# Optimization experiments

Hardware: AMD Instinct MI355X
Metric: run time of the kernel (lower is better)

The kernel has to match this reference:

```python
import jax, jax.numpy as jnp
import numpy as np

# ---- hardcoded module constants (from Cyborg.__init__) ----
B, S, V = 256, 128, 512
H = 30              # number of symbol vectors
N_STACKS = 2
R = 2               # REDUNDANCY
DEPTH = 4           # stack_depth
ZERO_OFFSET = 1e-6
NAND_BIAS = 3.0
INIT_SHARPEN = 10.0
N_VECS = 1 + N_STACKS  # input vec + one peek per stack = 3
C_BIG = (H + N_STACKS) * R   # 64 choices for push_fn / calc_out
C_SMALL = 2 * R              # 4 choices for pop_op / push_op


def _cossim(a, b, eps=1e-8):
    # torch.cosine_similarity semantics: per-vector norm clamp
    na = jnp.maximum(jnp.linalg.norm(a, axis=-1, keepdims=True), eps)
    nb = jnp.maximum(jnp.linalg.norm(b, axis=-1, keepdims=True), eps)
    return jnp.sum((a / na) * (b / nb), axis=-1)


def _nand(query, w, nw_raw):
    # Fuzzy-NAND gate bank (neurallambda NAND, clip='abs').
    # query: [B, N_VECS*V], w: [C, N_VECS*V], nw_raw: [C, N_VECS] -> [B, C]
    C = w.shape[0]
    q = query.reshape(-1, 1, N_VECS, V)
    wv = w.reshape(1, C, N_VECS, V)
    cos = jnp.abs(_cossim(q, wv))                 # [B, C, N_VECS], clip='abs'
    nw = jax.nn.sigmoid(nw_raw)[None]             # interpolate sim vs NOT(sim)
    interp = nw * cos + (1.0 - nw) * (1.0 - cos)
    return jnp.prod(interp, axis=-1)              # fuzzy AND over the 3 vecs


# ---- differentiable stack (soft pointer over DEPTH slots) ----
def _read(stack, ptr):
    return jnp.einsum('bdv,bd->bv', stack, ptr)

def _push(stack, ptr, val):
    p = jnp.roll(ptr, 1, axis=1)
    s = stack * (1.0 - p)[..., None] + val[:, None, :] * p[..., None]
    return s, p

def _pop(stack, ptr):
    s = stack * (1.0 - ptr)[..., None] + ZERO_OFFSET * ptr[..., None]
    p = jnp.roll(ptr, -1, axis=1)
    return s, p

def _pop_or_nop(stack, ptr, sharp, should_pop, should_nop):
    pr = jax.nn.softmax(jnp.stack([should_pop, should_nop], -1) * sharp, axis=-1)
    ps, pp = _pop(stack, ptr)
    s = ps * pr[:, 0, None, None] + stack * pr[:, 1, None, None]
    p = pp * pr[:, 0, None] + ptr * pr[:, 1, None]
    return s, p

def _push_or_nop(stack, ptr, sharp, should_push, should_nop, val):
    pr = jax.nn.softmax(jnp.stack([should_push, should_nop], -1) * sharp, axis=-1)
    ps, pp = _push(stack, ptr, val)
    s = ps * pr[:, 0, None, None] + stack * pr[:, 1, None, None]
    p = pp * pr[:, 0, None] + ptr * pr[:, 1, None]
    return s, p


def _forward(x, syms, stack_init_vec, sharp, pop_w, pop_nw, pushop_w, pushop_nw,
             pushfn_w, pushfn_nw, calc_w, calc_nw):
    b = x.shape[0]
    # init both stacks to zero_offset, pointer at slot 0, then hard-push init vec
    stack0 = jnp.full((N_STACKS, b, DEPTH, V), ZERO_OFFSET, x.dtype)
    ptr0 = jnp.zeros((N_STACKS, b, DEPTH), x.dtype).at[:, :, 0].set(1.0)
    init_val = jnp.broadcast_to(stack_init_vec, (b, V))
    stack0, ptr0 = jax.vmap(_push, in_axes=(0, 0, None))(stack0, ptr0, init_val)

    syms_b = jnp.broadcast_to(syms, (b, H, V))

    def step(carry, inp):
        stacks, ptrs = carry                                    # [2,B,D,V], [2,B,D]
        peeks = jax.vmap(_read)(stacks, ptrs)                   # [2,B,V]
        inps = jnp.concatenate([inp, peeks[0], peeks[1]], -1)   # [B,3V]
        out_opts = jnp.concatenate(
            [syms_b, peeks[0][:, None], peeks[1][:, None]], 1)  # [B,H+2,V]
        new_s, new_p = [], []
        for k in range(N_STACKS):
            pops = _nand(inps, pop_w[k], pop_nw[k])             # [B, 2R]
            pushes = _nand(inps, pushop_w[k], pushop_nw[k])     # [B, 2R]
            pv = _nand(inps, pushfn_w[k], pushfn_nw[k]).reshape(b, H + N_STACKS, R)
            push_val = jnp.einsum('bcv,bcr->bv', out_opts, pv)
            s, p = _pop_or_nop(stacks[k], ptrs[k], sharp[k],
                               pops[:, :R].max(1), pops[:, R:].max(1))
            s, p = _push_or_nop(s, p, sharp[k],
                                pushes[:, :R].max(1), pushes[:, R:].max(1), push_val)
            new_s.append(s)
            new_p.append(p)
        stacks = jnp.stack(new_s)
        ptrs = jnp.stack(new_p)
        peeks2 = jax.vmap(_read)(stacks, ptrs)
        inps2 = jnp.concatenate([inp, peeks2[0], peeks2[1]], -1)
        out_opts2 = jnp.concatenate(
            [syms_b, peeks2[0][:, None], peeks2[1][:, None]], 1)
        cv = _nand(inps2, calc_w, calc_nw).reshape(b, H + N_STACKS, R)
        out = jnp.einsum('bcv,bcr->bv', out_opts2, cv)
        return (stacks, ptrs), out

    _, outs = jax.lax.scan(step, (stack0, ptr0), jnp.swapaxes(x, 0, 1))
    return jnp.swapaxes(outs, 0, 1)  # [B,S,V]


def setup_inputs() -> dict:
    key = jax.random.key(0)
    ks = jax.random.split(key, 12)
    siv = jax.random.normal(ks[1], (V,), jnp.float32)
    siv = siv / jnp.linalg.norm(siv)
    return {
        'x': jax.random.normal(ks[0], (B, S, V), jnp.float32),
        'syms': jax.random.normal(ks[2], (H, V), jnp.float32),
        'stack_init_vec': siv,
        'sharp': jnp.full((N_STACKS,), INIT_SHARPEN, jnp.float32),
        'pop_w': jax.random.normal(ks[3], (N_STACKS, C_SMALL, N_VECS * V), jnp.float32),
        'pop_nw': jax.random.normal(ks[4], (N_STACKS, C_SMALL, N_VECS), jnp.float32) + NAND_BIAS,
        'pushop_w': jax.random.normal(ks[5], (N_STACKS, C_SMALL, N_VECS * V), jnp.float32),
        'pushop_nw': jax.random.normal(ks[6], (N_STACKS, C_SMALL, N_VECS), jnp.float32) + NAND_BIAS,
        'pushfn_w': jax.random.normal(ks[7], (N_STACKS, C_BIG, N_VECS * V), jnp.float32),
        'pushfn_nw': jax.random.normal(ks[8], (N_STACKS, C_BIG, N_VECS), jnp.float32) + NAND_BIAS,
        'calc_w': jax.random.normal(ks[9], (C_BIG, N_VECS * V), jnp.float32),
        'calc_nw': jax.random.normal(ks[10], (C_BIG, N_VECS), jnp.float32) + NAND_BIAS,
    }


def reference(x, syms, stack_init_vec, sharp, pop_w, pop_nw, pushop_w, pushop_nw,
              pushfn_w, pushfn_nw, calc_w, calc_nw):
    return _forward(x, syms, stack_init_vec, sharp, pop_w, pop_nw, pushop_w,
                    pushop_nw, pushfn_w, pushfn_nw, calc_w, calc_nw)
```

## Files before the change

kernel.cpp:

```cpp
#include <hip/hip_runtime.h>
#include <math.h>


#define SS 128
#define VV 512
#define NROWS 208
#define ZOFF 1e-6f

#define OFF_I0   0
#define OFF_OC   (32768*208)
#define OFF_GI   (OFF_OC + 32768*32)
#define OFF_M    (OFF_GI + 2*32*208)
#define OFF_A    (OFF_M + 1024)
#define OFF_Bc   (OFF_A + 624)
#define OFF_W0   (OFF_Bc + 624)

typedef _Float16 half8 __attribute__((ext_vector_type(8)));
typedef float f32x4 __attribute__((ext_vector_type(4)));

__device__ __forceinline__ float rlane(float v, int lane) {
    return __int_as_float(__builtin_amdgcn_readlane(__float_as_int(v), lane));
}
template <int CTRL>
__device__ __forceinline__ float dpp_add(float x) {
    int y = __builtin_amdgcn_update_dpp(0, __float_as_int(x), CTRL, 0xF, 0xF, true);
    return x + __int_as_float(y);
}
__device__ __forceinline__ float sum16(float x) {
    x = dpp_add<0xB1>(x);
    x = dpp_add<0x4E>(x);
    x = dpp_add<0x124>(x);
    x = dpp_add<0x128>(x);
    return x;
}
__device__ __forceinline__ float swz16(float x) {
    return __int_as_float(__builtin_amdgcn_ds_swizzle(__float_as_int(x), 0x401F));
}

__device__ __forceinline__ const float* w_row(int r, const float* pw, const float* pow_,
                                              const float* pfw, const float* cw) {
    if (r < 8)   return pw   + r * 1536;
    if (r < 16)  return pow_ + (r - 8) * 1536;
    if (r < 144) return pfw  + (r - 16) * 1536;
    return cw + (r - 144) * 1536;
}
__device__ __forceinline__ const float* nw_row(int r, const float* pn, const float* pon,
                                               const float* pfn, const float* cn) {
    if (r < 8)   return pn   + r * 3;
    if (r < 16)  return pon  + (r - 8) * 3;
    if (r < 144) return pfn  + (r - 16) * 3;
    return cn + (r - 144) * 3;
}

__global__ void kB(const float* __restrict__ syms, const float* __restrict__ siv,
                   const float* __restrict__ pw, const float* __restrict__ pn,
                   const float* __restrict__ pow_, const float* __restrict__ pon,
                   const float* __restrict__ pfw, const float* __restrict__ pfn,
                   const float* __restrict__ cw, const float* __restrict__ cn,
                   float* __restrict__ ws) {
    int blk = blockIdx.x, tid = threadIdx.x;
    if (blk < 64) {
        int jj = blk >> 5, e = blk & 31;
        __shared__ float bas[512];
        for (int i = tid; i < 512; i += 256)
            bas[i] = (e == 0) ? 1.0f : ((e == 1) ? siv[i] : syms[(e - 2) * 512 + i]);
        __syncthreads();
        if (tid < NROWS) {
            int c = tid;
            const float4* w4 = (const float4*)(w_row(c, pw, pow_, pfw, cw) + (jj + 1) * 512);
            const float4* b4 = (const float4*)bas;
            float s = 0.f;
            for (int q = 0; q < 128; ++q) {
                float4 a = b4[q], b = w4[q];
                s += a.x * b.x + a.y * b.y + a.z * b.z + a.w * b.w;
            }
            ws[OFF_GI + (jj * 32 + e) * 208 + c] = s;
        }
    } else if (blk == 64) {
        __shared__ float basw[32 * 512];
        for (int i = tid; i < 32 * 512; i += 256) {
            int m = i >> 9, v = i & 511;
            basw[i] = (m == 0) ? 1.0f : ((m == 1) ? siv[v] : syms[(m - 2) * 512 + v]);
        }
        __syncthreads();
        for (int p = tid; p < 1024; p += 256) {
            int m = p >> 5, mm = p & 31;
            const float4* a4 = (const float4*)(basw + m * 512);
            const float4* b4 = (const float4*)(basw + mm * 512);
            float s = 0.f;
            for (int q = 0; q < 128; ++q) {
                float4 a = a4[q], b = b4[q];
                s += a.x * b.x + a.y * b.y + a.z * b.z + a.w * b.w;
            }
            ws[OFF_M + p] = s;
        }
    } else if (blk == 65) {
        for (int idx = tid; idx < 624; idx += 256) {
            int r = idx / 3, j = idx % 3;
            const float4* w4 = (const float4*)(w_row(r, pw, pow_, pfw, cw) + j * 512);
            float s = 0.f;
            for (int q = 0; q < 128; ++q) {
                float4 b = w4[q];
                s += b.x * b.x + b.y * b.y + b.z * b.z + b.w * b.w;
            }
            float nrm = fmaxf(sqrtf(s), 1e-8f);
            float nwv = nw_row(r, pn, pon, pfn, cn)[j];
            float sig = 1.f / (1.f + expf(-nwv));
            ws[OFF_A + idx]  = (2.f * sig - 1.f) / nrm;
            ws[OFF_Bc + idx] = 1.f - sig;
        }
    } else {
        int part = blk - 66;
        _Float16* whp = (_Float16*)(ws + OFF_W0);
        _Float16* wlp = whp + 208 * 512;
        for (int i = tid; i < 6656; i += 256) {
            int flat = part * 6656 + i;
            int c = flat >> 9, v = flat & 511;
            float wv = w_row(c, pw, pow_, pfw, cw)[v];
            _Float16 h = (_Float16)wv;
            whp[flat] = h;
            wlp[flat] = (_Float16)(wv - (float)h);
        }
    }
}

__global__ __launch_bounds__(256) void kA(const float* __restrict__ x, float* __restrict__ ws) {
    __shared__ half8 AH[2][256];
    __shared__ half8 AL[2][256];
    __shared__ float red[256];
    __shared__ float invx[64];
    const int tid = threadIdx.x;
    const int wid = tid >> 6, l = tid & 63;
    const size_t bt0 = (size_t)blockIdx.x * 64;

    const int sr = tid >> 2, ss = tid & 3;
    const float* xp = x + (bt0 + sr) * 512 + ss * 8;
    const int wpos = (sr >> 4) * 64 + (sr & 15) + (ss << 4);

    const _Float16* whp = (const _Float16*)(ws + OFF_W0);
    const _Float16* wlp = whp + 208 * 512;

    const int t0 = (wid == 0) ? 0 : (1 + 3 * wid);
    const int nt = (wid == 0) ? 4 : 3;

    f32x4 acc[4][4];
#pragma unroll
    for (int m = 0; m < 4; ++m)
#pragma unroll
        for (int tt = 0; tt < 4; ++tt)
            acc[m][tt] = (f32x4){0.f, 0.f, 0.f, 0.f};

    float sumsq = 0.f;

    {
        float v[8];
        *(float4*)v       = *(const float4*)(xp);
        *(float4*)(v + 4) = *(const float4*)(xp + 4);
        half8 hh, hl;
#pragma unroll
        for (int j = 0; j < 8; ++j) {
            sumsq += v[j] * v[j];
            _Float16 h = (_Float16)v[j];
            hh[j] = h;
            hl[j] = (_Float16)(v[j] - (float)h);
        }
        AH[0][wpos] = hh;
        AL[0][wpos] = hl;
    }
    __syncthreads();

    for (int kt = 0; kt < 16; ++kt) {
        const int buf = kt & 1;
        half8 ahm[4], alm[4];
#pragma unroll
        for (int m = 0; m < 4; ++m) {
            ahm[m] = AH[buf][m * 64 + l];
            alm[m] = AL[buf][m * 64 + l];
        }
        float4 xv0, xv1;
        if (kt < 15) {
            xv0 = *(const float4*)(xp + (kt + 1) * 32);
            xv1 = *(const float4*)(xp + (kt + 1) * 32 + 4);
        }
        const int kof = kt * 32 + (l >> 4) * 8;
#pragma unroll
        for (int tt = 0; tt < 4; ++tt) {
            if (tt < nt) {
                const int c = (t0 + tt) * 16 + (l & 15);
                half8 bh = *(const half8*)(whp + c * 512 + kof);
                half8 bl = *(const half8*)(wlp + c * 512 + kof);
#pragma unroll
                for (int m = 0; m < 4; ++m) {
                    acc[m][tt] = __builtin_amdgcn_mfma_f32_16x16x32_f16(ahm[m], bh, acc[m][tt], 0, 0, 0);
                    acc[m][tt] = __builtin_amdgcn_mfma_f32_16x16x32_f16(ahm[m], bl, acc[m][tt], 0, 0, 0);
                    acc[m][tt] = __builtin_amdgcn_mfma_f32_16x16x32_f16(alm[m], bh, acc[m][tt], 0, 0, 0);
                }
            }
        }
        if (kt < 15) {
            float v[8];
            *(float4*)v = xv0; *(float4*)(v + 4) = xv1;
            half8 hh, hl;
#pragma unroll
            for (int j = 0; j < 8; ++j) {
                sumsq += v[j] * v[j];
                _Float16 h = (_Float16)v[j];
                hh[j] = h;
                hl[j] = (_Float16)(v[j] - (float)h);
            }
            AH[buf ^ 1][wpos] = hh;
            AL[buf ^ 1][wpos] = hl;
        }
        __syncthreads();
    }

    red[tid] = sumsq;
    __syncthreads();
    if (tid < 64) {
        float s = red[tid * 4] + red[tid * 4 + 1] + red[tid * 4 + 2] + red[tid * 4 + 3];
        invx[tid] = 1.f / fmaxf(sqrtf(s), 1e-8f);
    }
    __syncthreads();

#pragma unroll
    for (int tt = 0; tt < 4; ++tt) {
        if (tt < nt) {
            const int c = (t0 + tt) * 16 + (l & 15);
            const float A0 = ws[OFF_A + c * 3];
            const float B0 = ws[OFF_Bc + c * 3];
#pragma unroll
            for (int m = 0; m < 4; ++m) {
                const int rbase = m * 16 + (l >> 4) * 4;
#pragma unroll
                for (int j = 0; j < 4; ++j) {
                    const float ix = invx[rbase + j];
                    ws[OFF_I0 + (bt0 + rbase + j) * 208 + c] = A0 * fabsf(acc[m][tt][j]) * ix + B0;
                }
            }
        }
    }
}

__global__ __attribute__((amdgpu_flat_work_group_size(256, 256), amdgpu_waves_per_eu(1, 1)))
void kC(float* __restrict__ ws, const float* __restrict__ sharp) {
    __shared__ float nndL[2][144];
    const int b = blockIdx.x, tid = threadIdx.x;
    const int wid = tid >> 6, l = tid & 63;
    const int k = l >> 5, m = l & 31;
    const int isW3 = (wid == 3);
    const int isRow = (tid < 144);
    const int r = isW3 ? (144 + l) : tid;

    const float* GI = ws + OFF_GI;
    float G[64];
#pragma unroll
    for (int i = 0; i < 32; ++i) {
        G[i]      = GI[i * 208 + r];
        G[32 + i] = GI[(32 + i) * 208 + r];
    }
    const float A1 = ws[OFF_A + r * 3 + 1],  A2 = ws[OFF_A + r * 3 + 2];
    const float B1 = ws[OFF_Bc + r * 3 + 1], B2 = ws[OFF_Bc + r * 3 + 2];
    float Mrow[32];
#pragma unroll
    for (int q = 0; q < 8; ++q) {
        float4 mr = *(const float4*)(ws + OFF_M + m * 32 + 4 * q);
        Mrow[4*q] = mr.x; Mrow[4*q+1] = mr.y; Mrow[4*q+2] = mr.z; Mrow[4*q+3] = mr.w;
    }
    const float sh = sharp[k];

    float st[4], p[4];
#pragma unroll
    for (int d = 0; d < 4; ++d) {
        st[d] = (d == 1) ? ((m == 1) ? 1.f : 0.f) : ((m == 0) ? ZOFF : 0.f);
        p[d] = (d == 1) ? 1.f : 0.f;
    }
    float pk = st[0] * p[0] + st[1] * p[1] + st[2] * p[2] + st[3] * p[3];
    float pkOther = __shfl_xor(pk, 32);

    const float* i0base = ws + OFF_I0 + (size_t)b * SS * 208;
    const int ioff = isW3 ? 0 : 1;
    float i0pro = i0base[r];
    float i0use = i0base[(size_t)ioff * 208 + r];

    auto CA = [&](float pp, float po, float iv) -> float {
        float gq0a = 0.f, gq0b = 0.f, gq1a = 0.f, gq1b = 0.f;
        float d1a = 0.f, d1b = 0.f, d2a = 0.f, d2b = 0.f;
#pragma unroll
        for (int mm = 0; mm < 32; ++mm) {
            float v0 = rlane(pp, mm);
            float v1 = rlane(pp, 32 + mm);
            if (mm & 1) {
                gq0b += Mrow[mm] * v0;  gq1b += Mrow[mm] * v1;
                d1b  += G[mm] * v0;     d2b  += G[32 + mm] * v1;
            } else {
                gq0a += Mrow[mm] * v0;  gq1a += Mrow[mm] * v1;
                d1a  += G[mm] * v0;     d2a  += G[32 + mm] * v1;
            }
        }
        float pm0 = (k ? po : pp) * (gq0a + gq0b);
        float pm1 = (k ? pp : po) * (gq1a + gq1b);
        float q0 = sum16(pm0); q0 += swz16(q0);
        float q1 = sum16(pm1); q1 += swz16(q1);
        float iq0 = __frsqrt_rn(fmaxf(q0, 1e-16f));
        float iq1 = __frsqrt_rn(fmaxf(q1, 1e-16f));
        float dd1 = d1a + d1b, dd2 = d2a + d2b;
        return iv * (A1 * fabsf(dd1) * iq0 + B1) * (A2 * fabsf(dd2) * iq1 + B2);
    };

    {
        float nv0 = CA(pk, pkOther, i0pro);
        if (isRow) nndL[0][tid] = nv0;
    }
    __syncthreads();

    for (int t = 0; t < SS; ++t) {
        int nidx = t + 1 + ioff; if (nidx > SS - 1) nidx = SS - 1;
        float i0nxt = i0base[(size_t)nidx * 208 + r];

        const float* nb = nndL[t & 1];
        float4 gp4 = *(const float4*)(nb + 4 * k);
        float4 gq4 = *(const float4*)(nb + 8 + 4 * k);
        float prp0 = 1.f / (1.f + __expf((fmaxf(gp4.z, gp4.w) - fmaxf(gp4.x, gp4.y)) * sh));
        float prq0 = 1.f / (1.f + __expf((fmaxf(gq4.z, gq4.w) - fmaxf(gq4.x, gq4.y)) * sh));
        float prp1 = 1.f - prp0, prq1 = 1.f - prq0;
        float prx = 0.f, pry = 0.f;
        if (m >= 2) {
            float2 pr2 = *(const float2*)(nb + 16 + 64 * k + 2 * m - 4);
            prx = pr2.x; pry = pr2.y;
        }
        float4 t30 = *(const float4*)(nb + 16 + 64 * k + 60);
        float pk0m = k ? pkOther : pk;
        float pk1m = k ? pk : pkOther;
        float pvc = prx + pry + (t30.x + t30.y) * pk0m + (t30.z + t30.w) * pk1m;

        float zc = (m == 0) ? ZOFF : 0.f;
        float s1[4], p1[4];
#pragma unroll
        for (int d = 0; d < 4; ++d) {
            float ps = st[d] * (1.f - p[d]) + zc * p[d];
            s1[d] = ps * prp0 + st[d] * prp1;
            p1[d] = p[(d + 1) & 3] * prp0 + p[d] * prp1;
        }
#pragma unroll
        for (int d = 0; d < 4; ++d) {
            float pu = p1[(d + 3) & 3];
            float su = s1[d] * (1.f - pu) + pvc * pu;
            st[d] = su * prq0 + s1[d] * prq1;
            p[d] = pu * prq0 + p1[d] * prq1;
        }
        float pkp = st[0] * p[0] + st[1] * p[1] + st[2] * p[2] + st[3] * p[3];
        float pkpOth = __shfl_xor(pkp, 32);

        float nv = CA(pkp, pkpOth, i0use);
        if (isRow) nndL[(t + 1) & 1][tid] = nv;
        if (isW3) {
            float s60 = rlane(nv, 60), s61 = rlane(nv, 61);
            float s62 = rlane(nv, 62), s63 = rlane(nv, 63);
            int src = (m >= 2) ? (2 * m - 4) : 0;
            float cx = __shfl(nv, src);
            float cy = __shfl(nv, src + 1);
            if (m < 2) { cx = 0.f; cy = 0.f; }
            if (l < 32) {
                float oc = cx + cy + (s60 + s61) * pkp + (s62 + s63) * pkpOth;
                ws[OFF_OC + ((size_t)b * SS + t) * 32 + m] = oc;
            }
        }
        __syncthreads();
        pk = pkp;
        pkOther = pkpOth;
        i0use = i0nxt;
    }
}

__global__ __launch_bounds__(256) void kD(const float* __restrict__ ws, const float* __restrict__ syms,
                                          const float* __restrict__ siv, float* __restrict__ out) {
    int t = threadIdx.x;
    int rg = t >> 6;
    int vc = (t & 63) * 8;
    size_t r0 = (size_t)blockIdx.x * 16 + rg * 4;
    const float* oc = ws + OFF_OC;
    float acc[4][8];
    float4 sv0 = *(const float4*)(siv + vc);
    float4 sv1 = *(const float4*)(siv + vc + 4);
#pragma unroll
    for (int rr = 0; rr < 4; ++rr) {
        float c0 = oc[(r0 + rr) * 32 + 0];
        float c1 = oc[(r0 + rr) * 32 + 1];
        acc[rr][0] = c0 + c1 * sv0.x; acc[rr][1] = c0 + c1 * sv0.y;
        acc[rr][2] = c0 + c1 * sv0.z; acc[rr][3] = c0 + c1 * sv0.w;
        acc[rr][4] = c0 + c1 * sv1.x; acc[rr][5] = c0 + c1 * sv1.y;
        acc[rr][6] = c0 + c1 * sv1.z; acc[rr][7] = c0 + c1 * sv1.w;
    }
    for (int mm = 0; mm < 30; ++mm) {
        float4 b0 = *(const float4*)(syms + mm * 512 + vc);
        float4 b1 = *(const float4*)(syms + mm * 512 + vc + 4);
#pragma unroll
        for (int rr = 0; rr < 4; ++rr) {
            float c = oc[(r0 + rr) * 32 + 2 + mm];
            acc[rr][0] += c * b0.x; acc[rr][1] += c * b0.y;
            acc[rr][2] += c * b0.z; acc[rr][3] += c * b0.w;
            acc[rr][4] += c * b1.x; acc[rr][5] += c * b1.y;
            acc[rr][6] += c * b1.z; acc[rr][7] += c * b1.w;
        }
    }
#pragma unroll
    for (int rr = 0; rr < 4; ++rr) {
        float* o = out + (r0 + rr) * 512 + vc;
        *(float4*)o       = make_float4(acc[rr][0], acc[rr][1], acc[rr][2], acc[rr][3]);
        *(float4*)(o + 4) = make_float4(acc[rr][4], acc[rr][5], acc[rr][6], acc[rr][7]);
    }
}

extern "C" void kernel_launch(void* const* d_in, const int* in_sizes, int n_in,
                              void* d_out, int out_size, void* d_ws, size_t ws_size,
                              hipStream_t stream) {
    const float* x    = (const float*)d_in[0];
    const float* syms = (const float*)d_in[1];
    const float* siv  = (const float*)d_in[2];
    const float* shp  = (const float*)d_in[3];
    const float* pw   = (const float*)d_in[4];
    const float* pn   = (const float*)d_in[5];
    const float* pow_ = (const float*)d_in[6];
    const float* pon  = (const float*)d_in[7];
    const float* pfw  = (const float*)d_in[8];
    const float* pfn  = (const float*)d_in[9];
    const float* cw   = (const float*)d_in[10];
    const float* cn   = (const float*)d_in[11];
    float* ws  = (float*)d_ws;
    float* out = (float*)d_out;

    hipLaunchKernelGGL(kB, dim3(82),   dim3(256), 0, stream,
                       syms, siv, pw, pn, pow_, pon, pfw, pfn, cw, cn, ws);
    hipLaunchKernelGGL(kA, dim3(512),  dim3(256), 0, stream, x, ws);
    hipLaunchKernelGGL(kC, dim3(256),  dim3(256), 0, stream, ws, shp);
    hipLaunchKernelGGL(kD, dim3(2048), dim3(256), 0, stream, ws, syms, siv, out);
}
```

Baseline: 384.6 us.

## Load x directly into MFMA registers and use permlane32 swaps in recurrence

kA no longer stages the x tile through double-buffered LDS with a barrier per k-step. Each lane now loads its own A-fragment rows from global memory with register prefetch and computes row norms through swizzle and permlane reductions. In the serial recurrence kernel kC, the cross-half shuffles (__shfl_xor 32) are replaced by v_permlane32_swap. The 16-lane reduction is finished with readlanes instead of a swizzle. This removes LDS traffic and sync latency, at the cost of more global loads per lane and more registers.

```diff
diff --git a/kernel.cpp b/kernel.cpp
--- a/kernel.cpp
+++ b/kernel.cpp
@@ -35,6 +35,16 @@
 }
 __device__ __forceinline__ float swz16(float x) {
     return __int_as_float(__builtin_amdgcn_ds_swizzle(__float_as_int(x), 0x401F));
+}
+__device__ __forceinline__ void swap32(float x, float& lo, float& hi) {
+    float a = x, b = x;
+    asm("v_permlane32_swap_b32 %0, %1" : "+v"(a), "+v"(b));
+    lo = a; hi = b;
+}
+__device__ __forceinline__ float xor32(float x) {
+    float lo, hi;
+    swap32(x, lo, hi);
+    return (threadIdx.x & 32) ? lo : hi;
 }
 
 __device__ __forceinline__ const float* w_row(int r, const float* pw, const float* pow_,
@@ -125,17 +135,10 @@
 }
 
 __global__ __launch_bounds__(256) void kA(const float* __restrict__ x, float* __restrict__ ws) {
-    __shared__ half8 AH[2][256];
-    __shared__ half8 AL[2][256];
-    __shared__ float red[256];
-    __shared__ float invx[64];
     const int tid = threadIdx.x;
     const int wid = tid >> 6, l = tid & 63;
+    const int lr = l & 15, lk = l >> 4;
     const size_t bt0 = (size_t)blockIdx.x * 64;
-
-    const int sr = tid >> 2, ss = tid & 3;
-    const float* xp = x + (bt0 + sr) * 512 + ss * 8;
-    const int wpos = (sr >> 4) * 64 + (sr & 15) + (ss << 4);
 
     const _Float16* whp = (const _Float16*)(ws + OFF_W0);
     const _Float16* wlp = whp + 208 * 512;
@@ -150,90 +153,82 @@
         for (int tt = 0; tt < 4; ++tt)
             acc[m][tt] = (f32x4){0.f, 0.f, 0.f, 0.f};
 
-    float sumsq = 0.f;
-
-    {
-        float v[8];
-        *(float4*)v       = *(const float4*)(xp);
-        *(float4*)(v + 4) = *(const float4*)(xp + 4);
-        half8 hh, hl;
-#pragma unroll
-        for (int j = 0; j < 8; ++j) {
-            sumsq += v[j] * v[j];
-            _Float16 h = (_Float16)v[j];
-            hh[j] = h;
-            hl[j] = (_Float16)(v[j] - (float)h);
-        }
-        AH[0][wpos] = hh;
-        AL[0][wpos] = hl;
-    }
-    __syncthreads();
+    float sq[4] = {0.f, 0.f, 0.f, 0.f};
+    const float* xf = x + (bt0 + lr) * 512 + lk * 8;
+
+    float4 cur[4][2], nxt[4][2];
+#pragma unroll
+    for (int m = 0; m < 4; ++m) {
+        cur[m][0] = *(const float4*)(xf + m * 16 * 512);
+        cur[m][1] = *(const float4*)(xf + m * 16 * 512 + 4);
+    }
 
     for (int kt = 0; kt < 16; ++kt) {
-        const int buf = kt & 1;
-        half8 ahm[4], alm[4];
+        if (kt < 15) {
+#pragma unroll
+            for (int m = 0; m < 4; ++m) {
+                nxt[m][0] = *(const float4*)(xf + m * 16 * 512 + (kt + 1) * 32);
+                nxt[m][1] = *(const float4*)(xf + m * 16 * 512 + (kt + 1) * 32 + 4);
+            }
+        }
+        half8 ah[4], al[4];
 #pragma unroll
         for (int m = 0; m < 4; ++m) {
-            ahm[m] = AH[buf][m * 64 + l];
-            alm[m] = AL[buf][m * 64 + l];
-        }
-        float4 xv0, xv1;
-        if (kt < 15) {
-            xv0 = *(const float4*)(xp + (kt + 1) * 32);
-            xv1 = *(const float4*)(xp + (kt + 1) * 32 + 4);
-        }
-        const int kof = kt * 32 + (l >> 4) * 8;
-#pragma unroll
-        for (int tt = 0; tt < 4; ++tt) {
-            if (tt < nt) {
-                const int c = (t0 + tt) * 16 + (l & 15);
-                half8 bh = *(const half8*)(whp + c * 512 + kof);
-                half8 bl = *(const half8*)(wlp + c * 512 + kof);
-#pragma unroll
-                for (int m = 0; m < 4; ++m) {
-                    acc[m][tt] = __builtin_amdgcn_mfma_f32_16x16x32_f16(ahm[m], bh, acc[m][tt], 0, 0, 0);
-                    acc[m][tt] = __builtin_amdgcn_mfma_f32_16x16x32_f16(ahm[m], bl, acc[m][tt], 0, 0, 0);
-                    acc[m][tt] = __builtin_amdgcn_mfma_f32_16x16x32_f16(alm[m], bh, acc[m][tt], 0, 0, 0);
-                }
-            }
-        }
-        if (kt < 15) {
             float v[8];
-            *(float4*)v = xv0; *(float4*)(v + 4) = xv1;
+            *(float4*)v       = cur[m][0];
+            *(float4*)(v + 4) = cur[m][1];
             half8 hh, hl;
 #pragma unroll
             for (int j = 0; j < 8; ++j) {
-                sumsq += v[j] * v[j];
+                sq[m] += v[j] * v[j];
                 _Float16 h = (_Float16)v[j];
                 hh[j] = h;
                 hl[j] = (_Float16)(v[j] - (float)h);
             }
-            AH[buf ^ 1][wpos] = hh;
-            AL[buf ^ 1][wpos] = hl;
-        }
-        __syncthreads();
-    }
-
-    red[tid] = sumsq;
-    __syncthreads();
-    if (tid < 64) {
-        float s = red[tid * 4] + red[tid * 4 + 1] + red[tid * 4 + 2] + red[tid * 4 + 3];
-        invx[tid] = 1.f / fmaxf(sqrtf(s), 1e-8f);
-    }
-    __syncthreads();
+            ah[m] = hh; al[m] = hl;
+        }
+        const int kof = kt * 32 + lk * 8;
+#pragma unroll
+        for (int tt = 0; tt < 4; ++tt) {
+            if (tt < nt) {
+                const int c = (t0 + tt) * 16 + lr;
+                half8 bh = *(const half8*)(whp + c * 512 + kof);
+                half8 bl = *(const half8*)(wlp + c * 512 + kof);
+#pragma unroll
+                for (int m = 0; m < 4; ++m) {
+                    acc[m][tt] = __builtin_amdgcn_mfma_f32_16x16x32_f16(ah[m], bh, acc[m][tt], 0, 0, 0);
+                    acc[m][tt] = __builtin_amdgcn_mfma_f32_16x16x32_f16(ah[m], bl, acc[m][tt], 0, 0, 0);
+                    acc[m][tt] = __builtin_amdgcn_mfma_f32_16x16x32_f16(al[m], bh, acc[m][tt], 0, 0, 0);
+                }
+            }
+        }
+        if (kt < 15) {
+#pragma unroll
+            for (int m = 0; m < 4; ++m) { cur[m][0] = nxt[m][0]; cur[m][1] = nxt[m][1]; }
+        }
+    }
+
+    float ivx[4];
+#pragma unroll
+    for (int m = 0; m < 4; ++m) {
+        float rs = sq[m];
+        rs += swz16(rs);
+        rs += xor32(rs);
+        ivx[m] = __frsqrt_rn(fmaxf(rs, 1e-16f));
+    }
 
 #pragma unroll
     for (int tt = 0; tt < 4; ++tt) {
         if (tt < nt) {
-            const int c = (t0 + tt) * 16 + (l & 15);
+            const int c = (t0 + tt) * 16 + lr;
             const float A0 = ws[OFF_A + c * 3];
             const float B0 = ws[OFF_Bc + c * 3];
 #pragma unroll
             for (int m = 0; m < 4; ++m) {
-                const int rbase = m * 16 + (l >> 4) * 4;
+                const int rbase = m * 16 + lk * 4;
 #pragma unroll
                 for (int j = 0; j < 4; ++j) {
-                    const float ix = invx[rbase + j];
+                    const float ix = __shfl(ivx[m], lk * 4 + j);
                     ws[OFF_I0 + (bt0 + rbase + j) * 208 + c] = A0 * fabsf(acc[m][tt][j]) * ix + B0;
                 }
             }
@@ -275,14 +270,14 @@
         p[d] = (d == 1) ? 1.f : 0.f;
     }
     float pk = st[0] * p[0] + st[1] * p[1] + st[2] * p[2] + st[3] * p[3];
-    float pkOther = __shfl_xor(pk, 32);
+    float pkOther = xor32(pk);
 
     const float* i0base = ws + OFF_I0 + (size_t)b * SS * 208;
     const int ioff = isW3 ? 0 : 1;
     float i0pro = i0base[r];
     float i0use = i0base[(size_t)ioff * 208 + r];
 
-    auto CA = [&](float pp, float po, float iv) -> float {
+    auto CA = [&](float pp, float pk0v, float pk1v, float iv) -> float {
         float gq0a = 0.f, gq0b = 0.f, gq1a = 0.f, gq1b = 0.f;
         float d1a = 0.f, d1b = 0.f, d2a = 0.f, d2b = 0.f;
 #pragma unroll
@@ -297,10 +292,12 @@
                 d1a  += G[mm] * v0;     d2a  += G[32 + mm] * v1;
             }
         }
-        float pm0 = (k ? po : pp) * (gq0a + gq0b);
-        float pm1 = (k ? pp : po) * (gq1a + gq1b);
-        float q0 = sum16(pm0); q0 += swz16(q0);
-        float q1 = sum16(pm1); q1 += swz16(q1);
+        float pm0 = pk0v * (gq0a + gq0b);
+        float pm1 = pk1v * (gq1a + gq1b);
+        float s0 = sum16(pm0);
+        float s1 = sum16(pm1);
+        float q0 = rlane(s0, 0) + rlane(s0, 16);
+        float q1 = rlane(s1, 0) + rlane(s1, 16);
         float iq0 = __frsqrt_rn(fmaxf(q0, 1e-16f));
         float iq1 = __frsqrt_rn(fmaxf(q1, 1e-16f));
         float dd1 = d1a + d1b, dd2 = d2a + d2b;
@@ -308,7 +305,9 @@
     };
 
     {
-        float nv0 = CA(pk, pkOther, i0pro);
+        float lo0, hi0;
+        swap32(pk, lo0, hi0);
+        float nv0 = CA(pk, lo0, hi0, i0pro);
         if (isRow) nndL[0][tid] = nv0;
     }
     __syncthreads();
@@ -334,24 +333,26 @@
         float pvc = prx + pry + (t30.x + t30.y) * pk0m + (t30.z + t30.w) * pk1m;
 
         float zc = (m == 0) ? ZOFF : 0.f;
-        float s1[4], p1[4];
+        float s1v[4], p1[4];
 #pragma unroll
         for (int d = 0; d < 4; ++d) {
             float ps = st[d] * (1.f - p[d]) + zc * p[d];
-            s1[d] = ps * prp0 + st[d] * prp1;
+            s1v[d] = ps * prp0 + st[d] * prp1;
             p1[d] = p[(d + 1) & 3] * prp0 + p[d] * prp1;
         }
 #pragma unroll
         for (int d = 0; d < 4; ++d) {
             float pu = p1[(d + 3) & 3];
-            float su = s1[d] * (1.f - pu) + pvc * pu;
-            st[d] = su * prq0 + s1[d] * prq1;
+            float su = s1v[d] * (1.f - pu) + pvc * pu;
+            st[d] = su * prq0 + s1v[d] * prq1;
             p[d] = pu * prq0 + p1[d] * prq1;
         }
         float pkp = st[0] * p[0] + st[1] * p[1] + st[2] * p[2] + st[3] * p[3];
-        float pkpOth = __shfl_xor(pkp, 32);
-
-        float nv = CA(pkp, pkpOth, i0use);
+        float pk0v, pk1v;
+        swap32(pkp, pk0v, pk1v);
+        float pkpOth = k ? pk0v : pk1v;
+
+        float nv = CA(pkp, pk0v, pk1v, i0use);
         if (isRow) nndL[(t + 1) & 1][tid] = nv;
         if (isW3) {
             float s60 = rlane(nv, 60), s61 = rlane(nv, 61);
```

Measured after the change: 399.0 us. 1.04x slower.
